# Optimization experiments

Hardware: AMD Instinct MI355X
Metric: run time of the kernel (lower is better)

The kernel has to match this reference:

```python
import jax, jax.numpy as jnp
import numpy as np


def _squash(t):
    # squash along axis=2 (the atoms axis of [B, D, A, 1, 1])
    norm = jnp.linalg.norm(t, axis=2, keepdims=True)
    n2 = norm * norm
    return t / norm * (n2 / (1.0 + n2))


def setup_inputs() -> dict:
    key = jax.random.key(0)
    k1, k2 = jax.random.split(key)
    B, I, Ain, D, A = 32, 2048, 16, 32, 16
    x = jax.random.normal(k1, (B, I, Ain, 1, 1), jnp.float32)
    weights = 0.1 * jax.random.normal(k2, (I, Ain, D * A, 1, 1), jnp.float32)
    bias = jnp.full((D, A, 1, 1), 0.1, jnp.float32)  # nn.init.constant_(0.1)
    return {"x": x, "weights": weights, "bias": bias, "num_routing": 3}


def reference(x, weights, bias, num_routing):
    B, I, Ain = x.shape[:3]
    D, A = bias.shape[:2]
    # Vote computation (standard voting): sum over input_atoms.
    # Torch does expand+mul+sum; einsum is the same math without the 4.8GB intermediate.
    votes = jnp.einsum('bia,iao->bio', x[:, :, :, 0, 0],
                       weights[:, :, :, 0, 0]).reshape(B, I, D, A, 1, 1)
    votes_sg = jax.lax.stop_gradient(votes)  # votes_trans_stopped in torch
    logits = jnp.zeros((B, I, D, 1, 1), x.dtype)
    activation = None
    for i in range(num_routing):
        route = jax.nn.softmax(logits, axis=2)  # [B, I, D, 1, 1], softmax over D
        v = votes if i == num_routing - 1 else votes_sg
        # route broadcast over atoms axis; sum over input capsules I
        preact = jnp.sum(route[:, :, :, None] * v, axis=1) + bias  # [B, D, A, 1, 1]
        activation = _squash(preact)
        if i < num_routing - 1:
            # agreement update uses non-stopped votes (as in torch)
            logits = logits + jnp.sum(votes * activation[:, None], axis=3)  # [B, I, D, 1, 1]
    return activation
```

## Files before the change

### kernel.cpp

```cpp
#include <hip/hip_runtime.h>


#define B_  32
#define I_  2048
#define K_  16
#define O_  512
#define NG_ 256
#define IC_ 8

template<int PASS>
__global__ __launch_bounds__(256)
void sweep_kernel(const float* __restrict__ x, const float* __restrict__ W,
                  const float* __restrict__ act0_g, const float* __restrict__ act1_g,
                  float* __restrict__ partial)
{
    const int tid  = threadIdx.x;
    const int lane = tid & 63;
    const int wave = tid >> 6;
    const int ig   = blockIdx.x >> 1;
    const int bh   = blockIdx.x & 1;
    const int d    = lane >> 1;
    const int h    = lane & 1;
    const int obase = d * 16 + h * 8;

    const int wv   = __builtin_amdgcn_readfirstlane(wave);
    const int bbase = bh * 16 + wv * 4;

    __shared__ float sW[K_ * O_];

    float facc[4][8];
    #pragma unroll
    for (int bb = 0; bb < 4; ++bb)
        #pragma unroll
        for (int j = 0; j < 8; ++j) facc[bb][j] = 0.f;

    float a0[4][8], a1[4][8];
    if (PASS >= 1) {
        #pragma unroll
        for (int bb = 0; bb < 4; ++bb) {
            const float4* p = (const float4*)(act0_g + (bbase + bb) * O_ + obase);
            float4 f0 = p[0], f1 = p[1];
            a0[bb][0]=f0.x; a0[bb][1]=f0.y; a0[bb][2]=f0.z; a0[bb][3]=f0.w;
            a0[bb][4]=f1.x; a0[bb][5]=f1.y; a0[bb][6]=f1.z; a0[bb][7]=f1.w;
        }
    }
    if (PASS == 2) {
        #pragma unroll
        for (int bb = 0; bb < 4; ++bb) {
            const float4* p = (const float4*)(act1_g + (bbase + bb) * O_ + obase);
            float4 f0 = p[0], f1 = p[1];
            a1[bb][0]=f0.x; a1[bb][1]=f0.y; a1[bb][2]=f0.z; a1[bb][3]=f0.w;
            a1[bb][4]=f1.x; a1[bb][5]=f1.y; a1[bb][6]=f1.z; a1[bb][7]=f1.w;
        }
    }

    for (int ii = 0; ii < IC_; ++ii) {
        const int i = ig * IC_ + ii;
        __syncthreads();
        {
            const float4* Wg = (const float4*)(W + (size_t)i * (K_ * O_));
            #pragma unroll
            for (int q = 0; q < 8; ++q) {
                const int f  = tid + 256 * q;
                float4 w4 = Wg[f];
                const int e0 = 4 * f;
                const int k  = e0 >> 9;
                const int o  = e0 & (O_ - 1);
                const int dd = o >> 4;
                const int aa = o & 15;
                const int hh = aa >> 3;
                const int jq = (aa >> 2) & 1;
                *(float4*)&sW[jq * 4096 + k * 256 + (dd * 2 + hh) * 4] = w4;
            }
        }
        float xs[4][16];
        #pragma unroll
        for (int bb = 0; bb < 4; ++bb) {
            const float4* xp = (const float4*)(x + ((size_t)(bbase + bb) * I_ + i) * K_);
            #pragma unroll
            for (int q = 0; q < 4; ++q) {
                float4 v = xp[q];
                xs[bb][4*q+0]=v.x; xs[bb][4*q+1]=v.y; xs[bb][4*q+2]=v.z; xs[bb][4*q+3]=v.w;
            }
        }
        __syncthreads();

        float V[4][8];
        #pragma unroll
        for (int bb = 0; bb < 4; ++bb)
            #pragma unroll
            for (int j = 0; j < 8; ++j) V[bb][j] = 0.f;
        #pragma unroll
        for (int k = 0; k < K_; ++k) {
            const float4 w0 = *(const float4*)&sW[k * 256 + lane * 4];
            const float4 w1 = *(const float4*)&sW[4096 + k * 256 + lane * 4];
            const float w[8] = {w0.x, w0.y, w0.z, w0.w, w1.x, w1.y, w1.z, w1.w};
            #pragma unroll
            for (int bb = 0; bb < 4; ++bb) {
                const float xb = xs[bb][k];
                #pragma unroll
                for (int j = 0; j < 8; ++j) V[bb][j] = fmaf(xb, w[j], V[bb][j]);
            }
        }

        #pragma unroll
        for (int bb = 0; bb < 4; ++bb) {
            if (PASS == 0) {
                #pragma unroll
                for (int j = 0; j < 8; ++j) facc[bb][j] += V[bb][j];
            } else {
                float p0 = 0.f;
                #pragma unroll
                for (int j = 0; j < 8; ++j) p0 = fmaf(V[bb][j], a0[bb][j], p0);
                p0 += __shfl_xor(p0, 1);
                float lg = p0;
                if (PASS == 2) {
                    float p1 = 0.f;
                    #pragma unroll
                    for (int j = 0; j < 8; ++j) p1 = fmaf(V[bb][j], a1[bb][j], p1);
                    p1 += __shfl_xor(p1, 1);
                    lg += p1;
                }
                const float e = __expf(lg);
                float s = e;
                s += __shfl_xor(s, 2);
                s += __shfl_xor(s, 4);
                s += __shfl_xor(s, 8);
                s += __shfl_xor(s, 16);
                s += __shfl_xor(s, 32);
                const float r = e * __builtin_amdgcn_rcpf(s);
                #pragma unroll
                for (int j = 0; j < 8; ++j)
                    facc[bb][j] = fmaf(r, V[bb][j], facc[bb][j]);
            }
        }
    }

    #pragma unroll
    for (int bb = 0; bb < 4; ++bb) {
        const int b = bbase + bb;
        float4* dst = (float4*)(partial + ((size_t)ig * B_ + b) * O_ + obase);
        dst[0] = make_float4(facc[bb][0], facc[bb][1], facc[bb][2], facc[bb][3]);
        dst[1] = make_float4(facc[bb][4], facc[bb][5], facc[bb][6], facc[bb][7]);
    }
}

__global__ __launch_bounds__(256)
void reduce_squash(const float* __restrict__ partial, const float* __restrict__ bias,
                   float scale, float* __restrict__ out)
{
    const int t  = threadIdx.x;
    const int g  = blockIdx.x * 32 + (t & 31);
    const int sl = t >> 5;
    float s = 0.f;
    #pragma unroll
    for (int w = sl * 32; w < sl * 32 + 32; ++w)
        s += partial[(size_t)w * (B_ * O_) + g];
    __shared__ float red[256];
    red[t] = s;
    __syncthreads();
    if (t < 32) {
        float v = red[t];
        #pragma unroll
        for (int r = 1; r < 8; ++r) v += red[t + 32 * r];
        const float p = fmaf(v, scale, bias[g & (O_ - 1)]);
        float nn = p * p;
        nn += __shfl_xor(nn, 1);
        nn += __shfl_xor(nn, 2);
        nn += __shfl_xor(nn, 4);
        nn += __shfl_xor(nn, 8);
        out[g] = p * sqrtf(nn) / (1.f + nn);
    }
}

extern "C" void kernel_launch(void* const* d_in, const int* in_sizes, int n_in,
                              void* d_out, int out_size, void* d_ws, size_t ws_size,
                              hipStream_t stream) {
    const float* x    = (const float*)d_in[0];
    const float* W    = (const float*)d_in[1];
    const float* bias = (const float*)d_in[2];
    float* out = (float*)d_out;

    float* partial = (float*)d_ws;
    float* act0    = partial + (size_t)NG_ * B_ * O_;
    float* act1    = act0 + B_ * O_;

    sweep_kernel<0><<<NG_ * 2, 256, 0, stream>>>(x, W, nullptr, nullptr, partial);
    reduce_squash<<<512, 256, 0, stream>>>(partial, bias, 1.f / 32.f, act0);
    sweep_kernel<1><<<NG_ * 2, 256, 0, stream>>>(x, W, act0, nullptr, partial);
    reduce_squash<<<512, 256, 0, stream>>>(partial, bias, 1.f, act1);
    sweep_kernel<2><<<NG_ * 2, 256, 0, stream>>>(x, W, act0, act1, partial);
    reduce_squash<<<512, 256, 0, stream>>>(partial, bias, 1.f, out);
}
```

Baseline: 188.9 us.

## Double-buffer weight tiles with async global-to-LDS loads and XCD-aware block mapping

```diff
diff --git a/kernel.cpp b/kernel.cpp
--- a/kernel.cpp
+++ b/kernel.cpp
@@ -8,8 +8,11 @@
 #define NG_ 256
 #define IC_ 8
 
+#define GLB(p)  ((const __attribute__((address_space(1))) void*)(p))
+#define LDSP(p) ((__attribute__((address_space(3))) void*)(p))
+
 template<int PASS>
-__global__ __launch_bounds__(256)
+__global__ __launch_bounds__(256, 2)
 void sweep_kernel(const float* __restrict__ x, const float* __restrict__ W,
                   const float* __restrict__ act0_g, const float* __restrict__ act1_g,
                   float* __restrict__ partial)
@@ -17,16 +20,26 @@
     const int tid  = threadIdx.x;
     const int lane = tid & 63;
     const int wave = tid >> 6;
-    const int ig   = blockIdx.x >> 1;
-    const int bh   = blockIdx.x & 1;
+    const int bid  = blockIdx.x;
+    const int ig   = (bid & 7) * 32 + (bid >> 4);
+    const int bh   = (bid >> 3) & 1;
     const int d    = lane >> 1;
     const int h    = lane & 1;
     const int obase = d * 16 + h * 8;
 
-    const int wv   = __builtin_amdgcn_readfirstlane(wave);
+    const int wv    = __builtin_amdgcn_readfirstlane(wave);
     const int bbase = bh * 16 + wv * 4;
 
-    __shared__ float sW[K_ * O_];
+    __shared__ float sW[2][K_ * O_];
+
+    int voff[8];
+    #pragma unroll
+    for (int c = 0; c < 8; ++c) {
+        const int s = c * 256 + wave * 64 + lane;
+        const int f = ((s >> 10) & 1) | ((s & 1) << 1)
+                    | (((s >> 1) & 31) << 2) | (((s >> 6) & 15) << 7);
+        voff[c] = f << 4;
+    }
 
     float facc[4][8];
     #pragma unroll
@@ -54,25 +67,28 @@
         }
     }
 
+    {
+        const char* gb = (const char*)(W + (size_t)(ig * IC_) * (K_ * O_));
+        #pragma unroll
+        for (int c = 0; c < 8; ++c)
+            __builtin_amdgcn_global_load_lds(GLB(gb + voff[c]),
+                LDSP(&sW[0][(c * 256 + wave * 64) * 4]), 16, 0, 0);
+    }
+
+    #pragma unroll 1
     for (int ii = 0; ii < IC_; ++ii) {
         const int i = ig * IC_ + ii;
         __syncthreads();
-        {
-            const float4* Wg = (const float4*)(W + (size_t)i * (K_ * O_));
-            #pragma unroll
-            for (int q = 0; q < 8; ++q) {
-                const int f  = tid + 256 * q;
-                float4 w4 = Wg[f];
-                const int e0 = 4 * f;
-                const int k  = e0 >> 9;
-                const int o  = e0 & (O_ - 1);
-                const int dd = o >> 4;
-                const int aa = o & 15;
-                const int hh = aa >> 3;
-                const int jq = (aa >> 2) & 1;
-                *(float4*)&sW[jq * 4096 + k * 256 + (dd * 2 + hh) * 4] = w4;
-            }
-        }
+        if (ii + 1 < IC_) {
+            const char* gb = (const char*)(W + (size_t)(i + 1) * (K_ * O_));
+            float* nbuf = sW[(ii + 1) & 1];
+            #pragma unroll
+            for (int c = 0; c < 8; ++c)
+                __builtin_amdgcn_global_load_lds(GLB(gb + voff[c]),
+                    LDSP(&nbuf[(c * 256 + wave * 64) * 4]), 16, 0, 0);
+        }
+        const float* cbuf = sW[ii & 1];
+
         float xs[4][16];
         #pragma unroll
         for (int bb = 0; bb < 4; ++bb) {
@@ -83,7 +99,6 @@
                 xs[bb][4*q+0]=v.x; xs[bb][4*q+1]=v.y; xs[bb][4*q+2]=v.z; xs[bb][4*q+3]=v.w;
             }
         }
-        __syncthreads();
 
         float V[4][8];
         #pragma unroll
@@ -92,8 +107,8 @@
             for (int j = 0; j < 8; ++j) V[bb][j] = 0.f;
         #pragma unroll
         for (int k = 0; k < K_; ++k) {
-            const float4 w0 = *(const float4*)&sW[k * 256 + lane * 4];
-            const float4 w1 = *(const float4*)&sW[4096 + k * 256 + lane * 4];
+            const float4 w0 = *(const float4*)&cbuf[k * 256 + lane * 4];
+            const float4 w1 = *(const float4*)&cbuf[4096 + k * 256 + lane * 4];
             const float w[8] = {w0.x, w0.y, w0.z, w0.w, w1.x, w1.y, w1.z, w1.w};
             #pragma unroll
             for (int bb = 0; bb < 4; ++bb) {
```

Measured after the change: 188.8 us. About the same (-0.0%).

## Load weights directly from global memory, drop LDS staging, remap blocks

Applied to the files above, without the earlier changes.

```diff
diff --git a/kernel.cpp b/kernel.cpp
--- a/kernel.cpp
+++ b/kernel.cpp
@@ -9,7 +9,7 @@
 #define IC_ 8
 
 template<int PASS>
-__global__ __launch_bounds__(256)
+__global__ __launch_bounds__(256, 2)
 void sweep_kernel(const float* __restrict__ x, const float* __restrict__ W,
                   const float* __restrict__ act0_g, const float* __restrict__ act1_g,
                   float* __restrict__ partial)
@@ -17,16 +17,15 @@
     const int tid  = threadIdx.x;
     const int lane = tid & 63;
     const int wave = tid >> 6;
-    const int ig   = blockIdx.x >> 1;
-    const int bh   = blockIdx.x & 1;
+    const int bid  = blockIdx.x;
+    const int ig   = (bid & 7) * 32 + (bid >> 4);
+    const int bh   = (bid >> 3) & 1;
     const int d    = lane >> 1;
     const int h    = lane & 1;
     const int obase = d * 16 + h * 8;
 
-    const int wv   = __builtin_amdgcn_readfirstlane(wave);
+    const int wv    = __builtin_amdgcn_readfirstlane(wave);
     const int bbase = bh * 16 + wv * 4;
-
-    __shared__ float sW[K_ * O_];
 
     float facc[4][8];
     #pragma unroll
@@ -54,25 +53,12 @@
         }
     }
 
+    const float* Wl = W + (size_t)(ig * IC_) * (K_ * O_) + obase;
+
+    #pragma unroll 2
     for (int ii = 0; ii < IC_; ++ii) {
         const int i = ig * IC_ + ii;
-        __syncthreads();
-        {
-            const float4* Wg = (const float4*)(W + (size_t)i * (K_ * O_));
-            #pragma unroll
-            for (int q = 0; q < 8; ++q) {
-                const int f  = tid + 256 * q;
-                float4 w4 = Wg[f];
-                const int e0 = 4 * f;
-                const int k  = e0 >> 9;
-                const int o  = e0 & (O_ - 1);
-                const int dd = o >> 4;
-                const int aa = o & 15;
-                const int hh = aa >> 3;
-                const int jq = (aa >> 2) & 1;
-                *(float4*)&sW[jq * 4096 + k * 256 + (dd * 2 + hh) * 4] = w4;
-            }
-        }
+
         float xs[4][16];
         #pragma unroll
         for (int bb = 0; bb < 4; ++bb) {
@@ -83,8 +69,8 @@
                 xs[bb][4*q+0]=v.x; xs[bb][4*q+1]=v.y; xs[bb][4*q+2]=v.z; xs[bb][4*q+3]=v.w;
             }
         }
-        __syncthreads();
 
+        const float* Wi = Wl + (size_t)ii * (K_ * O_);
         float V[4][8];
         #pragma unroll
         for (int bb = 0; bb < 4; ++bb)
@@ -92,8 +78,8 @@
             for (int j = 0; j < 8; ++j) V[bb][j] = 0.f;
         #pragma unroll
         for (int k = 0; k < K_; ++k) {
-            const float4 w0 = *(const float4*)&sW[k * 256 + lane * 4];
-            const float4 w1 = *(const float4*)&sW[4096 + k * 256 + lane * 4];
+            const float4 w0 = *(const float4*)(Wi + k * O_);
+            const float4 w1 = *(const float4*)(Wi + k * O_ + 4);
             const float w[8] = {w0.x, w0.y, w0.z, w0.w, w1.x, w1.y, w1.z, w1.w};
             #pragma unroll
             for (int bb = 0; bb < 4; ++bb) {
```

After: 243.8 us. +29.1%, slower.
